# Kernel optimization log

Hardware: AMD Instinct MI355X
Metric: run time of the kernel (lower is better)

## Reference

```python
import jax, jax.numpy as jnp
import numpy as np

Q_DIM = 1024
K_DIM = 1024
V_DIM = 1024
ATTEN_DIM = 1024
NUM_HEADS = 16
HEAD_DIM = ATTEN_DIM // NUM_HEADS
B, L = 4, 2048


def setup_inputs() -> dict:
    key = jax.random.key(0)
    ks = jax.random.split(key, 11)
    s = 0.02
    return {
        "query": jax.random.normal(ks[0], (B, L, Q_DIM), dtype=jnp.float32),
        "key":   jax.random.normal(ks[1], (B, L, K_DIM), dtype=jnp.float32),
        "value": jax.random.normal(ks[2], (B, L, V_DIM), dtype=jnp.float32),
        "Wq": jax.random.normal(ks[3], (Q_DIM, ATTEN_DIM), dtype=jnp.float32) * s,
        "bq": jnp.zeros((ATTEN_DIM,), dtype=jnp.float32),
        "Wk": jax.random.normal(ks[4], (K_DIM, ATTEN_DIM), dtype=jnp.float32) * s,
        "bk": jnp.zeros((ATTEN_DIM,), dtype=jnp.float32),
        "Wv": jax.random.normal(ks[5], (V_DIM, ATTEN_DIM), dtype=jnp.float32) * s,
        "bv": jnp.zeros((ATTEN_DIM,), dtype=jnp.float32),
        "Wo": jax.random.normal(ks[6], (ATTEN_DIM, V_DIM), dtype=jnp.float32) * s,
        "bo": jnp.zeros((V_DIM,), dtype=jnp.float32),
    }


def reference(query, key, value, Wq, bq, Wk, bk, Wv, bv, Wo, bo):
    # QKV projections
    q = query @ Wq + bq        # [B, L, A]
    k = key   @ Wk + bk        # [B, L, A]
    v = value @ Wv + bv        # [B, L, A]
    # split heads: [B, L, H, D]
    def split_heads(x):
        return x.reshape(x.shape[:-1] + (NUM_HEADS, HEAD_DIM))
    q, k, v = split_heads(q), split_heads(k), split_heads(v)
    scale = 1.0 / (HEAD_DIM ** 0.5)
    # scores: [B, H, Lq, Lk]
    scores = jnp.einsum("bqhd,bkhd->bhqk", q, k) * scale
    attn = jax.nn.softmax(scores, axis=-1)
    out = jnp.einsum("bhqk,bkhd->bqhd", attn, v)  # [B, Lq, H, D]
    out = out.reshape(out.shape[0], out.shape[1], ATTEN_DIM)
    return out @ Wo + bo
```

## Files before the change

kernel.cpp:

```cpp
#include <hip/hip_runtime.h>
#include <stdint.h>

#define L_SEQ 2048
#define BATCH 4
#define ADIM  1024
#define NH    16
#define HD    64

typedef __attribute__((ext_vector_type(8))) short bf16x8;
typedef __attribute__((ext_vector_type(4))) float f32x4;
typedef __attribute__((ext_vector_type(16))) float f32x16;
typedef __attribute__((ext_vector_type(2))) int i32x2;

__device__ __forceinline__ short f2bf(float f) {
    union { float f; unsigned u; } x; x.f = f;
    unsigned r = x.u + 0x7fffu + ((x.u >> 16) & 1u);
    return (short)(r >> 16);
}

__device__ __forceinline__ void async_ld16(void* lds, const void* g) {
    __builtin_amdgcn_global_load_lds(
        (const __attribute__((address_space(1))) void*)g,
        (__attribute__((address_space(3))) void*)lds, 16, 0, 0);
}

__device__ __forceinline__ int cvtpk_bf16(float a, float b) {
    int r;
    asm("v_cvt_pk_bf16_f32 %0, %1, %2" : "=v"(r) : "v"(a), "v"(b));
    return r;
}

__device__ __forceinline__ bf16x8 pack4(int a, int b, int c, int d) {
    union { int i[4]; bf16x8 v; } u;
    u.i[0] = a; u.i[1] = b; u.i[2] = c; u.i[3] = d;
    return u.v;
}

__global__ void cvt3_kernel(const float* __restrict__ s0, const float* __restrict__ s1,
                            const float* __restrict__ s2, short* __restrict__ dst, int n4) {
    int i = blockIdx.x * blockDim.x + threadIdx.x;
    if (i >= n4) return;
    int z = blockIdx.y;
    const float* src = (z == 0) ? s0 : (z == 1) ? s1 : s2;
    float4 v = reinterpret_cast<const float4*>(src)[i];
    short4 s;
    s.x = f2bf(v.x); s.y = f2bf(v.y); s.z = f2bf(v.z); s.w = f2bf(v.w);
    reinterpret_cast<short4*>(dst + (size_t)z * (BATCH * L_SEQ * ADIM))[i] = s;
}

__global__ void transpose4_kernel(const float* __restrict__ W0, const float* __restrict__ W1,
                                  const float* __restrict__ W2, const float* __restrict__ W3,
                                  short* __restrict__ outb) {
    __shared__ float t[32][33];
    int z = blockIdx.z;
    const float* in = (z == 0) ? W0 : (z == 1) ? W1 : (z == 2) ? W2 : W3;
    short* out = outb + (size_t)z * (ADIM * ADIM);
    int x  = blockIdx.x * 32 + threadIdx.x;
    int y0 = blockIdx.y * 32 + threadIdx.y;
#pragma unroll
    for (int j = 0; j < 4; ++j)
        t[threadIdx.y + 8 * j][threadIdx.x] = in[(y0 + 8 * j) * 1024 + x];
    __syncthreads();
    int x2 = blockIdx.y * 32 + threadIdx.x;
    int y2 = blockIdx.x * 32 + threadIdx.y;
#pragma unroll
    for (int j = 0; j < 4; ++j)
        out[(y2 + 8 * j) * 1024 + x2] = f2bf(t[threadIdx.x][threadIdx.y + 8 * j]);
}

__device__ __forceinline__ void gemm_core(const short* __restrict__ A,
                                          const short* __restrict__ BT,
                                          const float* __restrict__ bias,
                                          void* __restrict__ Cout,
                                          int mode, float scalemul,
                                          int m0, int n0) {
    const int K = 1024, N = 1024;
    __shared__ __align__(16) short smem[16384];
    int tid = threadIdx.x;
    int wave = tid >> 6, lane = tid & 63, quad = lane >> 4, l16 = lane & 15;
    int wm = wave & 1, wn = wave >> 1;
    f32x4 acc[4][4] = {};

    int row = tid >> 2, ck = tid & 3;
    const short* gA0 = A  + (size_t)(m0 + row) * K + ck * 8;
    const short* gA1 = gA0 + (size_t)64 * K;
    const short* gB0 = BT + (size_t)(n0 + row) * K + ck * 8;
    const short* gB1 = gB0 + (size_t)64 * K;
    int loA0 = tid * 8, loA1 = tid * 8 + 2048;
    int loB0 = tid * 8 + 4096, loB1 = tid * 8 + 6144;

    async_ld16(smem + loA0, gA0); async_ld16(smem + loA1, gA1);
    async_ld16(smem + loB0, gB0); async_ld16(smem + loB1, gB1);
    gA0 += 32; gA1 += 32; gB0 += 32; gB1 += 32;
    __syncthreads();

    int cur = 0;
    for (int t = 0; t < 32; ++t) {
        if (t < 31) {
            int off = (cur ^ 1) * 8192;
            async_ld16(smem + off + loA0, gA0); async_ld16(smem + off + loA1, gA1);
            async_ld16(smem + off + loB0, gB0); async_ld16(smem + off + loB1, gB1);
            gA0 += 32; gA1 += 32; gB0 += 32; gB1 += 32;
        }
        const short* Ab = smem + cur * 8192;
        const short* Bb = Ab + 4096;
        bf16x8 af[4], bfr[4];
#pragma unroll
        for (int mt = 0; mt < 4; ++mt)
            af[mt] = *(const bf16x8*)&Ab[(wm * 64 + mt * 16 + l16) * 32 + quad * 8];
#pragma unroll
        for (int nt = 0; nt < 4; ++nt)
            bfr[nt] = *(const bf16x8*)&Bb[(wn * 64 + nt * 16 + l16) * 32 + quad * 8];
#pragma unroll
        for (int mt = 0; mt < 4; ++mt)
#pragma unroll
            for (int nt = 0; nt < 4; ++nt)
                acc[mt][nt] = __builtin_amdgcn_mfma_f32_16x16x32_bf16(
                    af[mt], bfr[nt], acc[mt][nt], 0, 0, 0);
        __syncthreads();
        cur ^= 1;
    }

    if (mode == 0) {
#pragma unroll
        for (int nt = 0; nt < 4; ++nt) {
            int col = n0 + wn * 64 + nt * 16 + l16;
            float bv = bias[col];
#pragma unroll
            for (int mt = 0; mt < 4; ++mt)
#pragma unroll
                for (int r = 0; r < 4; ++r) {
                    int rw = m0 + wm * 64 + mt * 16 + quad * 4 + r;
                    ((short*)Cout)[(size_t)rw * N + col] = f2bf((acc[mt][nt][r] + bv) * scalemul);
                }
        }
    } else if (mode == 1) {
#pragma unroll
        for (int nt = 0; nt < 4; ++nt) {
            int col = n0 + wn * 64 + nt * 16 + l16;
            float bv = bias[col];
            int h = col >> 6, d = col & 63;
#pragma unroll
            for (int mt = 0; mt < 4; ++mt)
#pragma unroll
                for (int r = 0; r < 4; ++r) {
                    int rw = m0 + wm * 64 + mt * 16 + quad * 4 + r;
                    int b = rw >> 11, lk = rw & 2047;
                    ((short*)Cout)[(((size_t)b * NH + h) * HD + d) * L_SEQ + lk] =
                        f2bf(acc[mt][nt][r] + bv);
                }
        }
    } else {
#pragma unroll
        for (int nt = 0; nt < 4; ++nt) {
            int col = n0 + wn * 64 + nt * 16 + l16;
            float bv = bias[col];
#pragma unroll
            for (int mt = 0; mt < 4; ++mt)
#pragma unroll
                for (int r = 0; r < 4; ++r) {
                    int rw = m0 + wm * 64 + mt * 16 + quad * 4 + r;
                    ((float*)Cout)[(size_t)rw * N + col] = acc[mt][nt][r] + bv;
                }
        }
    }
}

__device__ __forceinline__ void gemm_swz(int& m0, int& n0) {
    int bid = blockIdx.y * 8 + blockIdx.x;
    int swz = (bid & 7) * 64 + (bid >> 3);
    n0 = (swz & 7) * 128;
    m0 = (swz >> 3) * 128;
}

__global__ __launch_bounds__(256, 4)
void gemm_one(const short* __restrict__ A, const short* __restrict__ BT,
              const float* __restrict__ bias, void* __restrict__ Cout,
              int mode, float scalemul) {
    int m0, n0; gemm_swz(m0, n0);
    gemm_core(A, BT, bias, Cout, mode, scalemul, m0, n0);
}

__global__ __launch_bounds__(256, 4)
void qkv_gemm(const short* __restrict__ Xbase, const short* __restrict__ WTbase,
              const float* __restrict__ bq, const float* __restrict__ bk,
              const float* __restrict__ bv,
              short* __restrict__ Qb, short* __restrict__ Kb, short* __restrict__ VTout,
              float qscale) {
    int z = blockIdx.z;
    const short* A  = Xbase + (size_t)z * (BATCH * L_SEQ * ADIM);
    const short* BT = WTbase + (size_t)z * (ADIM * ADIM);
    const float* bias = (z == 0) ? bq : (z == 1) ? bk : bv;
    void* out = (z == 0) ? (void*)Qb : (z == 1) ? (void*)Kb : (void*)VTout;
    int mode = (z == 2) ? 1 : 0;
    float sm = (z == 0) ? qscale : 1.0f;
    int m0, n0; gemm_swz(m0, n0);
    gemm_core(A, BT, bias, out, mode, sm, m0, n0);
}

__global__ __launch_bounds__(256, 4)
void attn_kernel(const short* __restrict__ Qb, const short* __restrict__ Kb,
                 const short* __restrict__ VT, short* __restrict__ Oout) {
    __shared__ __align__(16) short lds[16384];
    int tid = threadIdx.x;
    int wave = tid >> 6, lane = tid & 63;
    int r31 = lane & 31, hi = lane >> 5;

    int f = (blockIdx.z * NH + blockIdx.y) * (L_SEQ / 128) + blockIdx.x;
    int swz = (f & 7) * 128 + (f >> 3);
    int qb = swz & 15;
    int h  = (swz >> 4) & 15;
    int b  = swz >> 8;

    size_t qrow = (size_t)(b * L_SEQ + qb * 128 + wave * 32 + r31) * ADIM + h * HD;
    bf16x8 qf[4];
#pragma unroll
    for (int dc = 0; dc < 4; ++dc)
        qf[dc] = *(const bf16x8*)&Qb[qrow + dc * 16 + hi * 8];

    const short* Kbase = Kb + (size_t)b * L_SEQ * ADIM + h * HD;
    const short* Vbase = VT + ((size_t)(b * NH + h) * HD) * L_SEQ;
    const short* gp[4]; int step[4]; int ldso[4];
#pragma unroll
    for (int s = 0; s < 4; ++s) {
        int j = s * 256 + tid;
        ldso[s] = j * 8;
        if (j < 512) {
            int row = j >> 3, c = (j & 7) ^ (row & 7);
            gp[s] = Kbase + (size_t)row * ADIM + c * 8;
            step[s] = 64 * ADIM;
        } else {
            int jv = j - 512;
            int row = jv >> 3, c = (jv & 7) ^ (row & 7);
            gp[s] = Vbase + (size_t)row * L_SEQ + c * 8;
            step[s] = 64;
        }
    }

    f32x16 o0 = {}, o1 = {};
    f32x4 lp = {};

#pragma unroll
    for (int s = 0; s < 4; ++s) { async_ld16(lds + ldso[s], gp[s]); gp[s] += step[s]; }
    __syncthreads();

    int cur = 0;
    for (int t = 0; t < 32; ++t) {
        const short* kb_l = lds + cur * 8192;
        const short* vb_l = kb_l + 4096;
        if (t < 31) {
            short* dst = lds + (cur ^ 1) * 8192;
#pragma unroll
            for (int s = 0; s < 4; ++s) { async_ld16(dst + ldso[s], gp[s]); gp[s] += step[s]; }
        }
#pragma unroll
        for (int kt = 0; kt < 2; ++kt) {
            const short* krow = kb_l + (kt * 32 + r31) * 64;
            f32x16 sv = {};
#pragma unroll
            for (int dc = 0; dc < 4; ++dc) {
                bf16x8 kf = *(const bf16x8*)&krow[((((dc << 1) + hi) ^ (r31 & 7)) << 3)];
                sv = __builtin_amdgcn_mfma_f32_32x32x16_bf16(kf, qf[dc], sv, 0, 0, 0);
            }
#pragma unroll
            for (int r = 0; r < 16; ++r) sv[r] = __builtin_amdgcn_exp2f(sv[r]);
#pragma unroll
            for (int m = 0; m < 4; ++m)
#pragma unroll
                for (int j2 = 0; j2 < 4; ++j2) lp[j2] += sv[m * 4 + j2];

            int p0 = cvtpk_bf16(sv[0],  sv[1]);
            int p1 = cvtpk_bf16(sv[2],  sv[3]);
            int p2 = cvtpk_bf16(sv[4],  sv[5]);
            int p3 = cvtpk_bf16(sv[6],  sv[7]);
            int p4 = cvtpk_bf16(sv[8],  sv[9]);
            int p5 = cvtpk_bf16(sv[10], sv[11]);
            int p6 = cvtpk_bf16(sv[12], sv[13]);
            int p7 = cvtpk_bf16(sv[14], sv[15]);
            asm volatile("v_permlane32_swap_b32 %0, %1" : "+v"(p0), "+v"(p2));
            asm volatile("v_permlane32_swap_b32 %0, %1" : "+v"(p1), "+v"(p3));
            asm volatile("v_permlane32_swap_b32 %0, %1" : "+v"(p4), "+v"(p6));
            asm volatile("v_permlane32_swap_b32 %0, %1" : "+v"(p5), "+v"(p7));
            bf16x8 pf0 = pack4(p0, p1, p2, p3);
            bf16x8 pf1 = pack4(p4, p5, p6, p7);

            const short* vrow = vb_l + r31 * 64;
#pragma unroll
            for (int dt = 0; dt < 2; ++dt) {
                const short* vr = vrow + dt * 2048;
                bf16x8 vf0 = *(const bf16x8*)&vr[((((kt << 2) + hi)     ^ (r31 & 7)) << 3)];
                bf16x8 vf1 = *(const bf16x8*)&vr[((((kt << 2) + 2 + hi) ^ (r31 & 7)) << 3)];
                if (dt == 0) {
                    o0 = __builtin_amdgcn_mfma_f32_32x32x16_bf16(vf0, pf0, o0, 0, 0, 0);
                    o0 = __builtin_amdgcn_mfma_f32_32x32x16_bf16(vf1, pf1, o0, 0, 0, 0);
                } else {
                    o1 = __builtin_amdgcn_mfma_f32_32x32x16_bf16(vf0, pf0, o1, 0, 0, 0);
                    o1 = __builtin_amdgcn_mfma_f32_32x32x16_bf16(vf1, pf1, o1, 0, 0, 0);
                }
            }
        }
        __syncthreads();
        cur ^= 1;
    }

    float lsum = lp[0] + lp[1] + lp[2] + lp[3];
    lsum += __shfl_xor(lsum, 32);
    float inv = __builtin_amdgcn_rcpf(lsum);

    short* tile = lds + wave * (32 * 68);
#pragma unroll
    for (int dt = 0; dt < 2; ++dt)
#pragma unroll
        for (int g = 0; g < 4; ++g) {
            int d0 = dt * 32 + g * 8 + hi * 4;
            int pa, pb;
            if (dt == 0) {
                pa = cvtpk_bf16(o0[g * 4 + 0] * inv, o0[g * 4 + 1] * inv);
                pb = cvtpk_bf16(o0[g * 4 + 2] * inv, o0[g * 4 + 3] * inv);
            } else {
                pa = cvtpk_bf16(o1[g * 4 + 0] * inv, o1[g * 4 + 1] * inv);
                pb = cvtpk_bf16(o1[g * 4 + 2] * inv, o1[g * 4 + 3] * inv);
            }
            *(i32x2*)&tile[r31 * 68 + d0] = (i32x2){pa, pb};
        }
    __syncthreads();
    size_t obase = (size_t)(b * L_SEQ + qb * 128 + wave * 32) * ADIM + h * HD;
    int rr = lane >> 3, cc = lane & 7;
#pragma unroll
    for (int p = 0; p < 4; ++p) {
        int row = p * 8 + rr;
        bf16x8 v = *(const bf16x8*)&tile[row * 68 + cc * 8];
        *(bf16x8*)&Oout[obase + (size_t)row * ADIM + cc * 8] = v;
    }
}

extern "C" void kernel_launch(void* const* d_in, const int* in_sizes, int n_in,
                              void* d_out, int out_size, void* d_ws, size_t ws_size,
                              hipStream_t stream) {
    const float* query = (const float*)d_in[0];
    const float* keyp  = (const float*)d_in[1];
    const float* value = (const float*)d_in[2];
    const float* Wq = (const float*)d_in[3];
    const float* bq = (const float*)d_in[4];
    const float* Wk = (const float*)d_in[5];
    const float* bk = (const float*)d_in[6];
    const float* Wv = (const float*)d_in[7];
    const float* bv = (const float*)d_in[8];
    const float* Wo = (const float*)d_in[9];
    const float* bo = (const float*)d_in[10];

    const float QSCALE = 0.125f * 1.44269504f;
    const size_t MB = 1ull << 20;
    const int n4 = (BATCH * L_SEQ * ADIM) / 4;
    char* w = (char*)d_ws;
    dim3 tblk(32, 8);
    dim3 gemm_grid(ADIM / 128, (BATCH * L_SEQ) / 128);
    dim3 attn_grid(L_SEQ / 128, NH, BATCH);

    if (ws_size >= 104 * MB) {
        short* X0  = (short*)(w);
        short* WT  = (short*)(w + 48 * MB);
        short* VT  = (short*)(w + 56 * MB);
        short* Kb  = (short*)(w + 72 * MB);
        short* Qb  = (short*)(w + 88 * MB);
        short* AO  = X0;

        cvt3_kernel<<<dim3(n4 / 256, 3), 256, 0, stream>>>(query, keyp, value, X0, n4);
        transpose4_kernel<<<dim3(32, 32, 4), tblk, 0, stream>>>(Wq, Wk, Wv, Wo, WT);
        qkv_gemm<<<dim3(ADIM / 128, (BATCH * L_SEQ) / 128, 3), 256, 0, stream>>>(
            X0, WT, bq, bk, bv, Qb, Kb, VT, QSCALE);
        attn_kernel<<<attn_grid, 256, 0, stream>>>(Qb, Kb, VT, AO);
        gemm_one<<<gemm_grid, 256, 0, stream>>>(AO, WT + (size_t)3 * ADIM * ADIM, bo,
                                                d_out, 2, 1.0f);
    } else {
        short* X0  = (short*)(w);
        short* WT  = (short*)(w + 16 * MB);
        short* VT  = (short*)(w + 24 * MB);
        short* Kb  = (short*)(w + 40 * MB);
        short* Qb  = (short*)(w + 56 * MB);

        transpose4_kernel<<<dim3(32, 32, 4), tblk, 0, stream>>>(Wq, Wk, Wv, Wo, WT);
        cvt3_kernel<<<dim3(n4 / 256, 1), 256, 0, stream>>>(query, query, query, X0, n4);
        gemm_one<<<gemm_grid, 256, 0, stream>>>(X0, WT, bq, Qb, 0, QSCALE);
        cvt3_kernel<<<dim3(n4 / 256, 1), 256, 0, stream>>>(keyp, keyp, keyp, X0, n4);
        gemm_one<<<gemm_grid, 256, 0, stream>>>(X0, WT + (size_t)ADIM * ADIM, bk, Kb, 0, 1.0f);
        cvt3_kernel<<<dim3(n4 / 256, 1), 256, 0, stream>>>(value, value, value, X0, n4);
        gemm_one<<<gemm_grid, 256, 0, stream>>>(X0, WT + (size_t)2 * ADIM * ADIM, bv, VT, 1, 1.0f);
        attn_kernel<<<attn_grid, 256, 0, stream>>>(Qb, Kb, VT, X0);
        gemm_one<<<gemm_grid, 256, 0, stream>>>(X0, WT + (size_t)3 * ADIM * ADIM, bo,
                                                d_out, 2, 1.0f);
    }
}
```

Measured before the change: 341.8 us.

## Process 64 query rows per wave in attention, halving block size

The attention kernel now runs 2 waves per block instead of 4, and each wave handles 64 query rows as two 32-row MFMA tiles. Each K and V fragment read from LDS is reused across both tiles, which halves LDS read traffic per MFMA, and the K/V tile loads are spread over 8 async loads per thread. MFMA sections are wrapped in s_setprio so matrix issue is favoured over other waves. The cost is roughly double the accumulator registers per wave and fewer waves per block, which can reduce occupancy and latency hiding, plus an extra barrier in the epilogue.

```diff
diff --git a/kernel.cpp b/kernel.cpp
--- a/kernel.cpp
+++ b/kernel.cpp
@@ -198,7 +198,7 @@
     gemm_core(A, BT, bias, out, mode, sm, m0, n0);
 }
 
-__global__ __launch_bounds__(256, 4)
+__global__ __launch_bounds__(128, 2)
 void attn_kernel(const short* __restrict__ Qb, const short* __restrict__ Kb,
                  const short* __restrict__ VT, short* __restrict__ Oout) {
     __shared__ __align__(16) short lds[16384];
@@ -212,18 +212,20 @@
     int h  = (swz >> 4) & 15;
     int b  = swz >> 8;
 
-    size_t qrow = (size_t)(b * L_SEQ + qb * 128 + wave * 32 + r31) * ADIM + h * HD;
-    bf16x8 qf[4];
-#pragma unroll
-    for (int dc = 0; dc < 4; ++dc)
-        qf[dc] = *(const bf16x8*)&Qb[qrow + dc * 16 + hi * 8];
+    size_t qbase = (size_t)(b * L_SEQ + qb * 128 + wave * 64) * ADIM + h * HD;
+    bf16x8 qf0[4], qf1[4];
+#pragma unroll
+    for (int dc = 0; dc < 4; ++dc) {
+        qf0[dc] = *(const bf16x8*)&Qb[qbase + (size_t)r31 * ADIM + dc * 16 + hi * 8];
+        qf1[dc] = *(const bf16x8*)&Qb[qbase + (size_t)(32 + r31) * ADIM + dc * 16 + hi * 8];
+    }
 
     const short* Kbase = Kb + (size_t)b * L_SEQ * ADIM + h * HD;
     const short* Vbase = VT + ((size_t)(b * NH + h) * HD) * L_SEQ;
-    const short* gp[4]; int step[4]; int ldso[4];
-#pragma unroll
-    for (int s = 0; s < 4; ++s) {
-        int j = s * 256 + tid;
+    const short* gp[8]; int step[8]; int ldso[8];
+#pragma unroll
+    for (int s = 0; s < 8; ++s) {
+        int j = s * 128 + tid;
         ldso[s] = j * 8;
         if (j < 512) {
             int row = j >> 3, c = (j & 7) ^ (row & 7);
@@ -237,11 +239,11 @@
         }
     }
 
-    f32x16 o0 = {}, o1 = {};
-    f32x4 lp = {};
-
-#pragma unroll
-    for (int s = 0; s < 4; ++s) { async_ld16(lds + ldso[s], gp[s]); gp[s] += step[s]; }
+    f32x16 o00 = {}, o01 = {}, o10 = {}, o11 = {};
+    f32x4 lp0 = {}, lp1 = {};
+
+#pragma unroll
+    for (int s = 0; s < 8; ++s) { async_ld16(lds + ldso[s], gp[s]); gp[s] += step[s]; }
     __syncthreads();
 
     int cur = 0;
@@ -251,86 +253,136 @@
         if (t < 31) {
             short* dst = lds + (cur ^ 1) * 8192;
 #pragma unroll
-            for (int s = 0; s < 4; ++s) { async_ld16(dst + ldso[s], gp[s]); gp[s] += step[s]; }
+            for (int s = 0; s < 8; ++s) { async_ld16(dst + ldso[s], gp[s]); gp[s] += step[s]; }
         }
 #pragma unroll
         for (int kt = 0; kt < 2; ++kt) {
             const short* krow = kb_l + (kt * 32 + r31) * 64;
-            f32x16 sv = {};
+            bf16x8 kf[4];
+#pragma unroll
+            for (int dc = 0; dc < 4; ++dc)
+                kf[dc] = *(const bf16x8*)&krow[((((dc << 1) + hi) ^ (r31 & 7)) << 3)];
+            f32x16 s0 = {}, s1 = {};
+            __builtin_amdgcn_s_setprio(1);
 #pragma unroll
             for (int dc = 0; dc < 4; ++dc) {
-                bf16x8 kf = *(const bf16x8*)&krow[((((dc << 1) + hi) ^ (r31 & 7)) << 3)];
-                sv = __builtin_amdgcn_mfma_f32_32x32x16_bf16(kf, qf[dc], sv, 0, 0, 0);
+                s0 = __builtin_amdgcn_mfma_f32_32x32x16_bf16(kf[dc], qf0[dc], s0, 0, 0, 0);
+                s1 = __builtin_amdgcn_mfma_f32_32x32x16_bf16(kf[dc], qf1[dc], s1, 0, 0, 0);
             }
-#pragma unroll
-            for (int r = 0; r < 16; ++r) sv[r] = __builtin_amdgcn_exp2f(sv[r]);
+            __builtin_amdgcn_s_setprio(0);
+
+#pragma unroll
+            for (int r = 0; r < 16; ++r) { s0[r] = __builtin_amdgcn_exp2f(s0[r]);
+                                           s1[r] = __builtin_amdgcn_exp2f(s1[r]); }
 #pragma unroll
             for (int m = 0; m < 4; ++m)
 #pragma unroll
-                for (int j2 = 0; j2 < 4; ++j2) lp[j2] += sv[m * 4 + j2];
-
-            int p0 = cvtpk_bf16(sv[0],  sv[1]);
-            int p1 = cvtpk_bf16(sv[2],  sv[3]);
-            int p2 = cvtpk_bf16(sv[4],  sv[5]);
-            int p3 = cvtpk_bf16(sv[6],  sv[7]);
-            int p4 = cvtpk_bf16(sv[8],  sv[9]);
-            int p5 = cvtpk_bf16(sv[10], sv[11]);
-            int p6 = cvtpk_bf16(sv[12], sv[13]);
-            int p7 = cvtpk_bf16(sv[14], sv[15]);
-            asm volatile("v_permlane32_swap_b32 %0, %1" : "+v"(p0), "+v"(p2));
-            asm volatile("v_permlane32_swap_b32 %0, %1" : "+v"(p1), "+v"(p3));
-            asm volatile("v_permlane32_swap_b32 %0, %1" : "+v"(p4), "+v"(p6));
-            asm volatile("v_permlane32_swap_b32 %0, %1" : "+v"(p5), "+v"(p7));
-            bf16x8 pf0 = pack4(p0, p1, p2, p3);
-            bf16x8 pf1 = pack4(p4, p5, p6, p7);
+                for (int j2 = 0; j2 < 4; ++j2) { lp0[j2] += s0[m * 4 + j2];
+                                                 lp1[j2] += s1[m * 4 + j2]; }
+
+            int a0 = cvtpk_bf16(s0[0],  s0[1]);
+            int a1 = cvtpk_bf16(s0[2],  s0[3]);
+            int a2 = cvtpk_bf16(s0[4],  s0[5]);
+            int a3 = cvtpk_bf16(s0[6],  s0[7]);
+            int a4 = cvtpk_bf16(s0[8],  s0[9]);
+            int a5 = cvtpk_bf16(s0[10], s0[11]);
+            int a6 = cvtpk_bf16(s0[12], s0[13]);
+            int a7 = cvtpk_bf16(s0[14], s0[15]);
+            asm volatile("v_permlane32_swap_b32 %0, %1" : "+v"(a0), "+v"(a2));
+            asm volatile("v_permlane32_swap_b32 %0, %1" : "+v"(a1), "+v"(a3));
+            asm volatile("v_permlane32_swap_b32 %0, %1" : "+v"(a4), "+v"(a6));
+            asm volatile("v_permlane32_swap_b32 %0, %1" : "+v"(a5), "+v"(a7));
+            bf16x8 pA0 = pack4(a0, a1, a2, a3);
+            bf16x8 pA1 = pack4(a4, a5, a6, a7);
+            int b0 = cvtpk_bf16(s1[0],  s1[1]);
+            int b1 = cvtpk_bf16(s1[2],  s1[3]);
+            int b2 = cvtpk_bf16(s1[4],  s1[5]);
+            int b3 = cvtpk_bf16(s1[6],  s1[7]);
+            int b4 = cvtpk_bf16(s1[8],  s1[9]);
+            int b5 = cvtpk_bf16(s1[10], s1[11]);
+            int b6 = cvtpk_bf16(s1[12], s1[13]);
+            int b7 = cvtpk_bf16(s1[14], s1[15]);
+            asm volatile("v_permlane32_swap_b32 %0, %1" : "+v"(b0), "+v"(b2));
+            asm volatile("v_permlane32_swap_b32 %0, %1" : "+v"(b1), "+v"(b3));
+            asm volatile("v_permlane32_swap_b32 %0, %1" : "+v"(b4), "+v"(b6));
+            asm volatile("v_permlane32_swap_b32 %0, %1" : "+v"(b5), "+v"(b7));
+            bf16x8 pB0 = pack4(b0, b1, b2, b3);
+            bf16x8 pB1 = pack4(b4, b5, b6, b7);
 
             const short* vrow = vb_l + r31 * 64;
-#pragma unroll
-            for (int dt = 0; dt < 2; ++dt) {
-                const short* vr = vrow + dt * 2048;
-                bf16x8 vf0 = *(const bf16x8*)&vr[((((kt << 2) + hi)     ^ (r31 & 7)) << 3)];
-                bf16x8 vf1 = *(const bf16x8*)&vr[((((kt << 2) + 2 + hi) ^ (r31 & 7)) << 3)];
-                if (dt == 0) {
-                    o0 = __builtin_amdgcn_mfma_f32_32x32x16_bf16(vf0, pf0, o0, 0, 0, 0);
-                    o0 = __builtin_amdgcn_mfma_f32_32x32x16_bf16(vf1, pf1, o0, 0, 0, 0);
-                } else {
-                    o1 = __builtin_amdgcn_mfma_f32_32x32x16_bf16(vf0, pf0, o1, 0, 0, 0);
-                    o1 = __builtin_amdgcn_mfma_f32_32x32x16_bf16(vf1, pf1, o1, 0, 0, 0);
-                }
-            }
+            bf16x8 vf00 = *(const bf16x8*)&vrow[((((kt << 2) + hi)     ^ (r31 & 7)) << 3)];
+            bf16x8 vf01 = *(const bf16x8*)&vrow[((((kt << 2) + 2 + hi) ^ (r31 & 7)) << 3)];
+            bf16x8 vf10 = *(const bf16x8*)&vrow[2048 + ((((kt << 2) + hi)     ^ (r31 & 7)) << 3)];
+            bf16x8 vf11 = *(const bf16x8*)&vrow[2048 + ((((kt << 2) + 2 + hi) ^ (r31 & 7)) << 3)];
+            __builtin_amdgcn_s_setprio(1);
+            o00 = __builtin_amdgcn_mfma_f32_32x32x16_bf16(vf00, pA0, o00, 0, 0, 0);
+            o10 = __builtin_amdgcn_mfma_f32_32x32x16_bf16(vf00, pB0, o10, 0, 0, 0);
+            o01 = __builtin_amdgcn_mfma_f32_32x32x16_bf16(vf10, pA0, o01, 0, 0, 0);
+            o11 = __builtin_amdgcn_mfma_f32_32x32x16_bf16(vf10, pB0, o11, 0, 0, 0);
+            o00 = __builtin_amdgcn_mfma_f32_32x32x16_bf16(vf01, pA1, o00, 0, 0, 0);
+            o10 = __builtin_amdgcn_mfma_f32_32x32x16_bf16(vf01, pB1, o10, 0, 0, 0);
+            o01 = __builtin_amdgcn_mfma_f32_32x32x16_bf16(vf11, pA1, o01, 0, 0, 0);
+            o11 = __builtin_amdgcn_mfma_f32_32x32x16_bf16(vf11, pB1, o11, 0, 0, 0);
+            __builtin_amdgcn_s_setprio(0);
         }
         __syncthreads();
         cur ^= 1;
     }
 
-    float lsum = lp[0] + lp[1] + lp[2] + lp[3];
-    lsum += __shfl_xor(lsum, 32);
-    float inv = __builtin_amdgcn_rcpf(lsum);
-
-    short* tile = lds + wave * (32 * 68);
-#pragma unroll
-    for (int dt = 0; dt < 2; ++dt)
-#pragma unroll
-        for (int g = 0; g < 4; ++g) {
-            int d0 = dt * 32 + g * 8 + hi * 4;
-            int pa, pb;
-            if (dt == 0) {
-                pa = cvtpk_bf16(o0[g * 4 + 0] * inv, o0[g * 4 + 1] * inv);
-                pb = cvtpk_bf16(o0[g * 4 + 2] * inv, o0[g * 4 + 3] * inv);
-            } else {
-                pa = cvtpk_bf16(o1[g * 4 + 0] * inv, o1[g * 4 + 1] * inv);
-                pb = cvtpk_bf16(o1[g * 4 + 2] * inv, o1[g * 4 + 3] * inv);
+    {
+        float lsum = lp0[0] + lp0[1] + lp0[2] + lp0[3];
+        lsum += __shfl_xor(lsum, 32);
+        float inv = __builtin_amdgcn_rcpf(lsum);
+        short* tile = lds + wave * (32 * 68);
+#pragma unroll
+        for (int dt = 0; dt < 2; ++dt)
+#pragma unroll
+            for (int g = 0; g < 4; ++g) {
+                int d0 = dt * 32 + g * 8 + hi * 4;
+                int pa, pb;
+                if (dt == 0) { pa = cvtpk_bf16(o00[g*4+0]*inv, o00[g*4+1]*inv);
+                               pb = cvtpk_bf16(o00[g*4+2]*inv, o00[g*4+3]*inv); }
+                else         { pa = cvtpk_bf16(o01[g*4+0]*inv, o01[g*4+1]*inv);
+                               pb = cvtpk_bf16(o01[g*4+2]*inv, o01[g*4+3]*inv); }
+                *(i32x2*)&tile[r31 * 68 + d0] = (i32x2){pa, pb};
             }
-            *(i32x2*)&tile[r31 * 68 + d0] = (i32x2){pa, pb};
-        }
+        __syncthreads();
+        size_t obase = (size_t)(b * L_SEQ + qb * 128 + wave * 64) * ADIM + h * HD;
+        int rr = lane >> 3, cc = lane & 7;
+#pragma unroll
+        for (int p = 0; p < 4; ++p) {
+            int row = p * 8 + rr;
+            bf16x8 v = *(const bf16x8*)&tile[row * 68 + cc * 8];
+            *(bf16x8*)&Oout[obase + (size_t)row * ADIM + cc * 8] = v;
+        }
+    }
     __syncthreads();
-    size_t obase = (size_t)(b * L_SEQ + qb * 128 + wave * 32) * ADIM + h * HD;
-    int rr = lane >> 3, cc = lane & 7;
-#pragma unroll
-    for (int p = 0; p < 4; ++p) {
-        int row = p * 8 + rr;
-        bf16x8 v = *(const bf16x8*)&tile[row * 68 + cc * 8];
-        *(bf16x8*)&Oout[obase + (size_t)row * ADIM + cc * 8] = v;
+    {
+        float lsum = lp1[0] + lp1[1] + lp1[2] + lp1[3];
+        lsum += __shfl_xor(lsum, 32);
+        float inv = __builtin_amdgcn_rcpf(lsum);
+        short* tile = lds + wave * (32 * 68);
+#pragma unroll
+        for (int dt = 0; dt < 2; ++dt)
+#pragma unroll
+            for (int g = 0; g < 4; ++g) {
+                int d0 = dt * 32 + g * 8 + hi * 4;
+                int pa, pb;
+                if (dt == 0) { pa = cvtpk_bf16(o10[g*4+0]*inv, o10[g*4+1]*inv);
+                               pb = cvtpk_bf16(o10[g*4+2]*inv, o10[g*4+3]*inv); }
+                else         { pa = cvtpk_bf16(o11[g*4+0]*inv, o11[g*4+1]*inv);
+                               pb = cvtpk_bf16(o11[g*4+2]*inv, o11[g*4+3]*inv); }
+                *(i32x2*)&tile[r31 * 68 + d0] = (i32x2){pa, pb};
+            }
+        __syncthreads();
+        size_t obase = (size_t)(b * L_SEQ + qb * 128 + wave * 64 + 32) * ADIM + h * HD;
+        int rr = lane >> 3, cc = lane & 7;
+#pragma unroll
+        for (int p = 0; p < 4; ++p) {
+            int row = p * 8 + rr;
+            bf16x8 v = *(const bf16x8*)&tile[row * 68 + cc * 8];
+            *(bf16x8*)&Oout[obase + (size_t)row * ADIM + cc * 8] = v;
+        }
     }
 }
 
@@ -369,7 +421,7 @@
         transpose4_kernel<<<dim3(32, 32, 4), tblk, 0, stream>>>(Wq, Wk, Wv, Wo, WT);
         qkv_gemm<<<dim3(ADIM / 128, (BATCH * L_SEQ) / 128, 3), 256, 0, stream>>>(
             X0, WT, bq, bk, bv, Qb, Kb, VT, QSCALE);
-        attn_kernel<<<attn_grid, 256, 0, stream>>>(Qb, Kb, VT, AO);
+        attn_kernel<<<attn_grid, 128, 0, stream>>>(Qb, Kb, VT, AO);
         gemm_one<<<gemm_grid, 256, 0, stream>>>(AO, WT + (size_t)3 * ADIM * ADIM, bo,
                                                 d_out, 2, 1.0f);
     } else {
@@ -386,7 +438,7 @@
         gemm_one<<<gemm_grid, 256, 0, stream>>>(X0, WT + (size_t)ADIM * ADIM, bk, Kb, 0, 1.0f);
         cvt3_kernel<<<dim3(n4 / 256, 1), 256, 0, stream>>>(value, value, value, X0, n4);
         gemm_one<<<gemm_grid, 256, 0, stream>>>(X0, WT + (size_t)2 * ADIM * ADIM, bv, VT, 1, 1.0f);
-        attn_kernel<<<attn_grid, 256, 0, stream>>>(Qb, Kb, VT, X0);
+        attn_kernel<<<attn_grid, 128, 0, stream>>>(Qb, Kb, VT, X0);
         gemm_one<<<gemm_grid, 256, 0, stream>>>(X0, WT + (size_t)3 * ADIM * ADIM, bo,
                                                 d_out, 2, 1.0f);
     }
```

New measurement: 331.1 us. 3.1% less time.

## Fuse fp32-to-bf16 input conversion into QKV GEMM and rework attention LDS layout

Applied to the files above, without the earlier changes.

Removes the separate cvt3 conversion kernel. The QKV GEMM now loads fp32 activations into registers, converts them to bf16, and writes them to LDS after the MFMA step, so it no longer reads and writes a bf16 copy of the inputs. The attention kernel's K/V LDS staging moves from an XOR-swizzled row layout to a chunk-major layout, adds s_setprio around the MFMA groups, and interleaves the o0/o1 MFMAs. The costs are more registers in the QKV GEMM (launch bounds drop to 3), fp32 A loads that no longer go through async LDS loads, and possible LDS bank-conflict changes from the new layout.

```diff
diff --git a/kernel.cpp b/kernel.cpp
--- a/kernel.cpp
+++ b/kernel.cpp
@@ -34,18 +34,6 @@
     union { int i[4]; bf16x8 v; } u;
     u.i[0] = a; u.i[1] = b; u.i[2] = c; u.i[3] = d;
     return u.v;
-}
-
-__global__ void cvt3_kernel(const float* __restrict__ s0, const float* __restrict__ s1,
-                            const float* __restrict__ s2, short* __restrict__ dst, int n4) {
-    int i = blockIdx.x * blockDim.x + threadIdx.x;
-    if (i >= n4) return;
-    int z = blockIdx.y;
-    const float* src = (z == 0) ? s0 : (z == 1) ? s1 : s2;
-    float4 v = reinterpret_cast<const float4*>(src)[i];
-    short4 s;
-    s.x = f2bf(v.x); s.y = f2bf(v.y); s.z = f2bf(v.z); s.w = f2bf(v.w);
-    reinterpret_cast<short4*>(dst + (size_t)z * (BATCH * L_SEQ * ADIM))[i] = s;
 }
 
 __global__ void transpose4_kernel(const float* __restrict__ W0, const float* __restrict__ W1,
@@ -68,7 +56,8 @@
         out[(y2 + 8 * j) * 1024 + x2] = f2bf(t[threadIdx.x][threadIdx.y + 8 * j]);
 }
 
-__device__ __forceinline__ void gemm_core(const short* __restrict__ A,
+template<int AFP32>
+__device__ __forceinline__ void gemm_core(const void* __restrict__ Aptr,
                                           const short* __restrict__ BT,
                                           const float* __restrict__ bias,
                                           void* __restrict__ Cout,
@@ -82,25 +71,52 @@
     f32x4 acc[4][4] = {};
 
     int row = tid >> 2, ck = tid & 3;
-    const short* gA0 = A  + (size_t)(m0 + row) * K + ck * 8;
-    const short* gA1 = gA0 + (size_t)64 * K;
     const short* gB0 = BT + (size_t)(n0 + row) * K + ck * 8;
     const short* gB1 = gB0 + (size_t)64 * K;
     int loA0 = tid * 8, loA1 = tid * 8 + 2048;
     int loB0 = tid * 8 + 4096, loB1 = tid * 8 + 6144;
 
-    async_ld16(smem + loA0, gA0); async_ld16(smem + loA1, gA1);
+    const short* gA0 = nullptr; const short* gA1 = nullptr;
+    const float* fA0 = nullptr; const float* fA1 = nullptr;
+    if (AFP32) {
+        fA0 = (const float*)Aptr + (size_t)(m0 + row) * K + ck * 8;
+        fA1 = fA0 + (size_t)64 * K;
+    } else {
+        gA0 = (const short*)Aptr + (size_t)(m0 + row) * K + ck * 8;
+        gA1 = gA0 + (size_t)64 * K;
+    }
+
+    if (AFP32) {
+        float4 x0 = *(const float4*)fA0, x1 = *(const float4*)(fA0 + 4);
+        float4 y0 = *(const float4*)fA1, y1 = *(const float4*)(fA1 + 4);
+        fA0 += 32; fA1 += 32;
+        *(bf16x8*)&smem[loA0] = pack4(cvtpk_bf16(x0.x, x0.y), cvtpk_bf16(x0.z, x0.w),
+                                      cvtpk_bf16(x1.x, x1.y), cvtpk_bf16(x1.z, x1.w));
+        *(bf16x8*)&smem[loA1] = pack4(cvtpk_bf16(y0.x, y0.y), cvtpk_bf16(y0.z, y0.w),
+                                      cvtpk_bf16(y1.x, y1.y), cvtpk_bf16(y1.z, y1.w));
+    } else {
+        async_ld16(smem + loA0, gA0); async_ld16(smem + loA1, gA1);
+        gA0 += 32; gA1 += 32;
+    }
     async_ld16(smem + loB0, gB0); async_ld16(smem + loB1, gB1);
-    gA0 += 32; gA1 += 32; gB0 += 32; gB1 += 32;
+    gB0 += 32; gB1 += 32;
     __syncthreads();
 
     int cur = 0;
     for (int t = 0; t < 32; ++t) {
+        float4 x0, x1, y0, y1;
         if (t < 31) {
             int off = (cur ^ 1) * 8192;
-            async_ld16(smem + off + loA0, gA0); async_ld16(smem + off + loA1, gA1);
+            if (AFP32) {
+                x0 = *(const float4*)fA0; x1 = *(const float4*)(fA0 + 4);
+                y0 = *(const float4*)fA1; y1 = *(const float4*)(fA1 + 4);
+                fA0 += 32; fA1 += 32;
+            } else {
+                async_ld16(smem + off + loA0, gA0); async_ld16(smem + off + loA1, gA1);
+                gA0 += 32; gA1 += 32;
+            }
             async_ld16(smem + off + loB0, gB0); async_ld16(smem + off + loB1, gB1);
-            gA0 += 32; gA1 += 32; gB0 += 32; gB1 += 32;
+            gB0 += 32; gB1 += 32;
         }
         const short* Ab = smem + cur * 8192;
         const short* Bb = Ab + 4096;
@@ -117,6 +133,13 @@
             for (int nt = 0; nt < 4; ++nt)
                 acc[mt][nt] = __builtin_amdgcn_mfma_f32_16x16x32_bf16(
                     af[mt], bfr[nt], acc[mt][nt], 0, 0, 0);
+        if (AFP32 && t < 31) {
+            int off = (cur ^ 1) * 8192;
+            *(bf16x8*)&smem[off + loA0] = pack4(cvtpk_bf16(x0.x, x0.y), cvtpk_bf16(x0.z, x0.w),
+                                                cvtpk_bf16(x1.x, x1.y), cvtpk_bf16(x1.z, x1.w));
+            *(bf16x8*)&smem[off + loA1] = pack4(cvtpk_bf16(y0.x, y0.y), cvtpk_bf16(y0.z, y0.w),
+                                                cvtpk_bf16(y1.x, y1.y), cvtpk_bf16(y1.z, y1.w));
+        }
         __syncthreads();
         cur ^= 1;
     }
@@ -178,24 +201,25 @@
               const float* __restrict__ bias, void* __restrict__ Cout,
               int mode, float scalemul) {
     int m0, n0; gemm_swz(m0, n0);
-    gemm_core(A, BT, bias, Cout, mode, scalemul, m0, n0);
-}
-
-__global__ __launch_bounds__(256, 4)
-void qkv_gemm(const short* __restrict__ Xbase, const short* __restrict__ WTbase,
+    gemm_core<0>(A, BT, bias, Cout, mode, scalemul, m0, n0);
+}
+
+__global__ __launch_bounds__(256, 3)
+void qkv_gemm(const float* __restrict__ Xq, const float* __restrict__ Xk,
+              const float* __restrict__ Xv, const short* __restrict__ WTbase,
               const float* __restrict__ bq, const float* __restrict__ bk,
               const float* __restrict__ bv,
               short* __restrict__ Qb, short* __restrict__ Kb, short* __restrict__ VTout,
               float qscale) {
     int z = blockIdx.z;
-    const short* A  = Xbase + (size_t)z * (BATCH * L_SEQ * ADIM);
+    const float* A = (z == 0) ? Xq : (z == 1) ? Xk : Xv;
     const short* BT = WTbase + (size_t)z * (ADIM * ADIM);
     const float* bias = (z == 0) ? bq : (z == 1) ? bk : bv;
     void* out = (z == 0) ? (void*)Qb : (z == 1) ? (void*)Kb : (void*)VTout;
     int mode = (z == 2) ? 1 : 0;
     float sm = (z == 0) ? qscale : 1.0f;
     int m0, n0; gemm_swz(m0, n0);
-    gemm_core(A, BT, bias, out, mode, sm, m0, n0);
+    gemm_core<1>(A, BT, bias, out, mode, sm, m0, n0);
 }
 
 __global__ __launch_bounds__(256, 4)
@@ -226,13 +250,13 @@
         int j = s * 256 + tid;
         ldso[s] = j * 8;
         if (j < 512) {
-            int row = j >> 3, c = (j & 7) ^ (row & 7);
-            gp[s] = Kbase + (size_t)row * ADIM + c * 8;
+            int c = j >> 6, k = j & 63;
+            gp[s] = Kbase + (size_t)k * ADIM + c * 8;
             step[s] = 64 * ADIM;
         } else {
             int jv = j - 512;
-            int row = jv >> 3, c = (jv & 7) ^ (row & 7);
-            gp[s] = Vbase + (size_t)row * L_SEQ + c * 8;
+            int c = jv >> 6, d = jv & 63;
+            gp[s] = Vbase + (size_t)d * L_SEQ + c * 8;
             step[s] = 64;
         }
     }
@@ -255,13 +279,14 @@
         }
 #pragma unroll
         for (int kt = 0; kt < 2; ++kt) {
-            const short* krow = kb_l + (kt * 32 + r31) * 64;
             f32x16 sv = {};
+            __builtin_amdgcn_s_setprio(1);
 #pragma unroll
             for (int dc = 0; dc < 4; ++dc) {
-                bf16x8 kf = *(const bf16x8*)&krow[((((dc << 1) + hi) ^ (r31 & 7)) << 3)];
+                bf16x8 kf = *(const bf16x8*)&kb_l[(((dc << 1) + hi) * 64 + kt * 32 + r31) * 8];
                 sv = __builtin_amdgcn_mfma_f32_32x32x16_bf16(kf, qf[dc], sv, 0, 0, 0);
             }
+            __builtin_amdgcn_s_setprio(0);
 #pragma unroll
             for (int r = 0; r < 16; ++r) sv[r] = __builtin_amdgcn_exp2f(sv[r]);
 #pragma unroll
@@ -284,20 +309,16 @@
             bf16x8 pf0 = pack4(p0, p1, p2, p3);
             bf16x8 pf1 = pack4(p4, p5, p6, p7);
 
-            const short* vrow = vb_l + r31 * 64;
-#pragma unroll
-            for (int dt = 0; dt < 2; ++dt) {
-                const short* vr = vrow + dt * 2048;
-                bf16x8 vf0 = *(const bf16x8*)&vr[((((kt << 2) + hi)     ^ (r31 & 7)) << 3)];
-                bf16x8 vf1 = *(const bf16x8*)&vr[((((kt << 2) + 2 + hi) ^ (r31 & 7)) << 3)];
-                if (dt == 0) {
-                    o0 = __builtin_amdgcn_mfma_f32_32x32x16_bf16(vf0, pf0, o0, 0, 0, 0);
-                    o0 = __builtin_amdgcn_mfma_f32_32x32x16_bf16(vf1, pf1, o0, 0, 0, 0);
-                } else {
-                    o1 = __builtin_amdgcn_mfma_f32_32x32x16_bf16(vf0, pf0, o1, 0, 0, 0);
-                    o1 = __builtin_amdgcn_mfma_f32_32x32x16_bf16(vf1, pf1, o1, 0, 0, 0);
-                }
-            }
+            bf16x8 vf00 = *(const bf16x8*)&vb_l[((kt * 4 + hi)     * 64 + r31) * 8];
+            bf16x8 vf01 = *(const bf16x8*)&vb_l[((kt * 4 + 2 + hi) * 64 + r31) * 8];
+            bf16x8 vf10 = *(const bf16x8*)&vb_l[((kt * 4 + hi)     * 64 + 32 + r31) * 8];
+            bf16x8 vf11 = *(const bf16x8*)&vb_l[((kt * 4 + 2 + hi) * 64 + 32 + r31) * 8];
+            __builtin_amdgcn_s_setprio(1);
+            o0 = __builtin_amdgcn_mfma_f32_32x32x16_bf16(vf00, pf0, o0, 0, 0, 0);
+            o1 = __builtin_amdgcn_mfma_f32_32x32x16_bf16(vf10, pf0, o1, 0, 0, 0);
+            o0 = __builtin_amdgcn_mfma_f32_32x32x16_bf16(vf01, pf1, o0, 0, 0, 0);
+            o1 = __builtin_amdgcn_mfma_f32_32x32x16_bf16(vf11, pf1, o1, 0, 0, 0);
+            __builtin_amdgcn_s_setprio(0);
         }
         __syncthreads();
         cur ^= 1;
@@ -351,43 +372,21 @@
 
     const float QSCALE = 0.125f * 1.44269504f;
     const size_t MB = 1ull << 20;
-    const int n4 = (BATCH * L_SEQ * ADIM) / 4;
     char* w = (char*)d_ws;
     dim3 tblk(32, 8);
     dim3 gemm_grid(ADIM / 128, (BATCH * L_SEQ) / 128);
     dim3 attn_grid(L_SEQ / 128, NH, BATCH);
 
-    if (ws_size >= 104 * MB) {
-        short* X0  = (short*)(w);
-        short* WT  = (short*)(w + 48 * MB);
-        short* VT  = (short*)(w + 56 * MB);
-        short* Kb  = (short*)(w + 72 * MB);
-        short* Qb  = (short*)(w + 88 * MB);
-        short* AO  = X0;
-
-        cvt3_kernel<<<dim3(n4 / 256, 3), 256, 0, stream>>>(query, keyp, value, X0, n4);
-        transpose4_kernel<<<dim3(32, 32, 4), tblk, 0, stream>>>(Wq, Wk, Wv, Wo, WT);
-        qkv_gemm<<<dim3(ADIM / 128, (BATCH * L_SEQ) / 128, 3), 256, 0, stream>>>(
-            X0, WT, bq, bk, bv, Qb, Kb, VT, QSCALE);
-        attn_kernel<<<attn_grid, 256, 0, stream>>>(Qb, Kb, VT, AO);
-        gemm_one<<<gemm_grid, 256, 0, stream>>>(AO, WT + (size_t)3 * ADIM * ADIM, bo,
-                                                d_out, 2, 1.0f);
-    } else {
-        short* X0  = (short*)(w);
-        short* WT  = (short*)(w + 16 * MB);
-        short* VT  = (short*)(w + 24 * MB);
-        short* Kb  = (short*)(w + 40 * MB);
-        short* Qb  = (short*)(w + 56 * MB);
-
-        transpose4_kernel<<<dim3(32, 32, 4), tblk, 0, stream>>>(Wq, Wk, Wv, Wo, WT);
-        cvt3_kernel<<<dim3(n4 / 256, 1), 256, 0, stream>>>(query, query, query, X0, n4);
-        gemm_one<<<gemm_grid, 256, 0, stream>>>(X0, WT, bq, Qb, 0, QSCALE);
-        cvt3_kernel<<<dim3(n4 / 256, 1), 256, 0, stream>>>(keyp, keyp, keyp, X0, n4);
-        gemm_one<<<gemm_grid, 256, 0, stream>>>(X0, WT + (size_t)ADIM * ADIM, bk, Kb, 0, 1.0f);
-        cvt3_kernel<<<dim3(n4 / 256, 1), 256, 0, stream>>>(value, value, value, X0, n4);
-        gemm_one<<<gemm_grid, 256, 0, stream>>>(X0, WT + (size_t)2 * ADIM * ADIM, bv, VT, 1, 1.0f);
-        attn_kernel<<<attn_grid, 256, 0, stream>>>(Qb, Kb, VT, X0);
-        gemm_one<<<gemm_grid, 256, 0, stream>>>(X0, WT + (size_t)3 * ADIM * ADIM, bo,
-                                                d_out, 2, 1.0f);
-    }
-}
+    short* AO = (short*)(w);
+    short* WT = (short*)(w + 16 * MB);
+    short* VT = (short*)(w + 24 * MB);
+    short* Kb = (short*)(w + 40 * MB);
+    short* Qb = (short*)(w + 56 * MB);
+
+    transpose4_kernel<<<dim3(32, 32, 4), tblk, 0, stream>>>(Wq, Wk, Wv, Wo, WT);
+    qkv_gemm<<<dim3(ADIM / 128, (BATCH * L_SEQ) / 128, 3), 256, 0, stream>>>(
+        query, keyp, value, WT, bq, bk, bv, Qb, Kb, VT, QSCALE);
+    attn_kernel<<<attn_grid, 256, 0, stream>>>(Qb, Kb, VT, AO);
+    gemm_one<<<gemm_grid, 256, 0, stream>>>(AO, WT + (size_t)3 * ADIM * ADIM, bo,
+                                            d_out, 2, 1.0f);
+}
```

Result: slower. 385.5 us (+12.8%).

## Use chunk-major LDS layout for K/V tiles, add MFMA priority hints

Applied to the files above, without the earlier changes.

Changes the LDS layout of the K and V tiles from an XOR-swizzled row-major layout to a chunk-major one, where the 8-element column chunk is the outer index and the row is the inner index. Lanes reading the same chunk across consecutive rows then hit contiguous 16-byte slots, which removes the swizzle arithmetic and aims to avoid bank conflicts. It also wraps the MFMA groups in s_setprio so waves issuing matrix ops get scheduling priority, and it interleaves the o0/o1 accumulations so back-to-back MFMAs are independent. The global-to-LDS copy pattern changes too: each group of 64 lanes now loads the same column chunk from 64 different rows, which may coalesce global reads less well.

```diff
diff --git a/kernel.cpp b/kernel.cpp
--- a/kernel.cpp
+++ b/kernel.cpp
@@ -226,13 +226,13 @@
         int j = s * 256 + tid;
         ldso[s] = j * 8;
         if (j < 512) {
-            int row = j >> 3, c = (j & 7) ^ (row & 7);
-            gp[s] = Kbase + (size_t)row * ADIM + c * 8;
+            int c = j >> 6, k = j & 63;
+            gp[s] = Kbase + (size_t)k * ADIM + c * 8;
             step[s] = 64 * ADIM;
         } else {
             int jv = j - 512;
-            int row = jv >> 3, c = (jv & 7) ^ (row & 7);
-            gp[s] = Vbase + (size_t)row * L_SEQ + c * 8;
+            int c = jv >> 6, d = jv & 63;
+            gp[s] = Vbase + (size_t)d * L_SEQ + c * 8;
             step[s] = 64;
         }
     }
@@ -255,13 +255,14 @@
         }
 #pragma unroll
         for (int kt = 0; kt < 2; ++kt) {
-            const short* krow = kb_l + (kt * 32 + r31) * 64;
             f32x16 sv = {};
+            __builtin_amdgcn_s_setprio(1);
 #pragma unroll
             for (int dc = 0; dc < 4; ++dc) {
-                bf16x8 kf = *(const bf16x8*)&krow[((((dc << 1) + hi) ^ (r31 & 7)) << 3)];
+                bf16x8 kf = *(const bf16x8*)&kb_l[(((dc << 1) + hi) * 64 + kt * 32 + r31) * 8];
                 sv = __builtin_amdgcn_mfma_f32_32x32x16_bf16(kf, qf[dc], sv, 0, 0, 0);
             }
+            __builtin_amdgcn_s_setprio(0);
 #pragma unroll
             for (int r = 0; r < 16; ++r) sv[r] = __builtin_amdgcn_exp2f(sv[r]);
 #pragma unroll
@@ -284,20 +285,16 @@
             bf16x8 pf0 = pack4(p0, p1, p2, p3);
             bf16x8 pf1 = pack4(p4, p5, p6, p7);
 
-            const short* vrow = vb_l + r31 * 64;
-#pragma unroll
-            for (int dt = 0; dt < 2; ++dt) {
-                const short* vr = vrow + dt * 2048;
-                bf16x8 vf0 = *(const bf16x8*)&vr[((((kt << 2) + hi)     ^ (r31 & 7)) << 3)];
-                bf16x8 vf1 = *(const bf16x8*)&vr[((((kt << 2) + 2 + hi) ^ (r31 & 7)) << 3)];
-                if (dt == 0) {
-                    o0 = __builtin_amdgcn_mfma_f32_32x32x16_bf16(vf0, pf0, o0, 0, 0, 0);
-                    o0 = __builtin_amdgcn_mfma_f32_32x32x16_bf16(vf1, pf1, o0, 0, 0, 0);
-                } else {
-                    o1 = __builtin_amdgcn_mfma_f32_32x32x16_bf16(vf0, pf0, o1, 0, 0, 0);
-                    o1 = __builtin_amdgcn_mfma_f32_32x32x16_bf16(vf1, pf1, o1, 0, 0, 0);
-                }
-            }
+            bf16x8 vf00 = *(const bf16x8*)&vb_l[((kt * 4 + hi)     * 64 + r31) * 8];
+            bf16x8 vf01 = *(const bf16x8*)&vb_l[((kt * 4 + 2 + hi) * 64 + r31) * 8];
+            bf16x8 vf10 = *(const bf16x8*)&vb_l[((kt * 4 + hi)     * 64 + 32 + r31) * 8];
+            bf16x8 vf11 = *(const bf16x8*)&vb_l[((kt * 4 + 2 + hi) * 64 + 32 + r31) * 8];
+            __builtin_amdgcn_s_setprio(1);
+            o0 = __builtin_amdgcn_mfma_f32_32x32x16_bf16(vf00, pf0, o0, 0, 0, 0);
+            o1 = __builtin_amdgcn_mfma_f32_32x32x16_bf16(vf10, pf0, o1, 0, 0, 0);
+            o0 = __builtin_amdgcn_mfma_f32_32x32x16_bf16(vf01, pf1, o0, 0, 0, 0);
+            o1 = __builtin_amdgcn_mfma_f32_32x32x16_bf16(vf11, pf1, o1, 0, 0, 0);
+            __builtin_amdgcn_s_setprio(0);
         }
         __syncthreads();
         cur ^= 1;
```

New measurement: 333.7 us. 1.02x faster.
